# Optimization experiments

Measured on AMD Instinct MI355X. Metric: run time of the kernel, lower is better.

Reference implementation:

```python
import jax, jax.numpy as jnp
import numpy as np

B, T, D, H, F, E, K = 4, 1024, 1024, 16, 2048, 8, 2
LN_EPS = 1e-6  # flax LayerNorm default


def setup_inputs() -> dict:
    key = jax.random.key(0)
    ks = jax.random.split(key, 8)
    s = 0.02
    return {
        "x": jax.random.normal(ks[0], (B, T, D), jnp.float32),
        "ln1_scale": jnp.ones((D,), jnp.float32),
        "ln1_bias": jnp.zeros((D,), jnp.float32),
        "qkv_w": jax.random.normal(ks[1], (D, 3 * D), jnp.float32) * s,
        "qkv_b": jnp.zeros((3 * D,), jnp.float32),
        "out_w": jax.random.normal(ks[2], (D, D), jnp.float32) * s,
        "out_b": jnp.zeros((D,), jnp.float32),
        "ln2_scale": jnp.ones((D,), jnp.float32),
        "ln2_bias": jnp.zeros((D,), jnp.float32),
        "router_w": jax.random.normal(ks[3], (D, E), jnp.float32) * s,
        "w1": jax.random.normal(ks[4], (E, D, F), jnp.float32) * s,
        "b1": jnp.zeros((E, F), jnp.float32),
        "w2": jax.random.normal(ks[5], (E, F, D), jnp.float32) * s,
        "b2": jnp.zeros((E, D), jnp.float32),
    }


def _layernorm(x, scale, bias):
    mu = jnp.mean(x, axis=-1, keepdims=True)
    var = jnp.mean(jnp.square(x - mu), axis=-1, keepdims=True)
    return (x - mu) * jax.lax.rsqrt(var + LN_EPS) * scale + bias


def _attention(x, qkv_w, qkv_b, out_w, out_b):
    b, t, d = x.shape
    hd = d // H
    qkv = x @ qkv_w + qkv_b
    q, k, v = jnp.split(qkv, 3, axis=-1)
    q = q.reshape(b, t, H, hd).transpose(0, 2, 1, 3)  # (B,H,T,hd)
    k = k.reshape(b, t, H, hd).transpose(0, 2, 1, 3)
    v = v.reshape(b, t, H, hd).transpose(0, 2, 1, 3)
    scale = jnp.sqrt(jnp.float32(hd))
    scores = jnp.einsum("bhqd,bhkd->bhqk", q, k) / scale
    causal = jnp.triu(jnp.ones((t, t), jnp.bool_), k=1)
    scores = jnp.where(causal[None, None], -1e9, scores)
    attn = jax.nn.softmax(scores, axis=-1)
    out = jnp.einsum("bhqk,bhkd->bhqd", attn, v)
    out = out.transpose(0, 2, 1, 3).reshape(b, t, d)
    return out @ out_w + out_b


def _moe(x, router_w, w1, b1, w2, b2):
    b, t, d = x.shape
    logits = x @ router_w  # (B,T,E)
    probs = jax.nn.softmax(logits, axis=-1)
    topk_vals, topk_idx = jax.lax.top_k(logits, K)  # (B,T,K)
    gates = jax.nn.softmax(topk_vals, axis=-1)
    # aux load-balancing loss from top-1 dispatch
    dispatch = jax.nn.one_hot(topk_idx[..., 0], E, dtype=x.dtype)
    f = jnp.mean(dispatch, axis=(0, 1))
    P = jnp.mean(probs, axis=(0, 1))
    aux_loss = E * jnp.sum(f * P)
    # dense all-expert compute (faithful to original)
    h = jax.nn.gelu(jnp.einsum("btd,edf->ebtf", x, w1) + b1[:, None, None, :])
    eo = jnp.einsum("ebtf,efd->ebtd", h, w2) + b2[:, None, None, :]  # (E,B,T,D)
    bi = jnp.arange(b)[:, None, None]
    ti = jnp.arange(t)[None, :, None]
    selected = eo[topk_idx, bi, ti, :]  # (B,T,K,D)
    out = jnp.sum(gates[..., None] * selected, axis=2)
    return out, aux_loss


def reference(x, ln1_scale, ln1_bias, qkv_w, qkv_b, out_w, out_b,
              ln2_scale, ln2_bias, router_w, w1, b1, w2, b2):
    res = x
    h = _layernorm(x, ln1_scale, ln1_bias)
    h = _attention(h, qkv_w, qkv_b, out_w, out_b)
    x = h + res
    res = x
    hn = _layernorm(x, ln2_scale, ln2_bias)
    moe_out, aux_loss = _moe(hn, router_w, w1, b1, w2, b2)
    return moe_out + res, aux_loss
```

## Files before the change

kernel.cpp:

```cpp
#include <hip/hip_runtime.h>
#include <hip/hip_bf16.h>

using bf16 = __hip_bfloat16;
typedef __attribute__((ext_vector_type(8))) short short8;
typedef __attribute__((ext_vector_type(4))) float f32x4;

__device__ __forceinline__ unsigned short f2bu(float x) {
  union { bf16 b; unsigned short u; } cv; cv.b = __float2bfloat16(x); return cv.u;
}

__device__ __forceinline__ void gload_lds16(const bf16* g, bf16* l) {
  __builtin_amdgcn_global_load_lds(
      (const __attribute__((address_space(1))) void*)g,
      (__attribute__((address_space(3))) void*)l, 16, 0, 0);
}

__global__ __launch_bounds__(256) void transpose_to_bf16(
    const float* __restrict__ in, bf16* __restrict__ out, int R, int C) {
  __shared__ float tile[64][65];
  size_t bo = (size_t)blockIdx.z * R * C;
  in += bo; out += bo;
  int c0 = blockIdx.x * 64, r0 = blockIdx.y * 64;
  int tx = threadIdx.x & 15, ty = threadIdx.x >> 4;
#pragma unroll
  for (int i = 0; i < 4; ++i) {
    float4 v = *(const float4*)&in[(size_t)(r0 + ty + i * 16) * C + c0 + tx * 4];
    tile[ty + i * 16][tx * 4 + 0] = v.x;
    tile[ty + i * 16][tx * 4 + 1] = v.y;
    tile[ty + i * 16][tx * 4 + 2] = v.z;
    tile[ty + i * 16][tx * 4 + 3] = v.w;
  }
  __syncthreads();
  int c = threadIdx.x >> 2;
  int rg = (threadIdx.x & 3) * 16;
#pragma unroll
  for (int j = 0; j < 4; ++j) {
    ushort4 o;
    o.x = f2bu(tile[rg + j * 4 + 0][c]);
    o.y = f2bu(tile[rg + j * 4 + 1][c]);
    o.z = f2bu(tile[rg + j * 4 + 2][c]);
    o.w = f2bu(tile[rg + j * 4 + 3][c]);
    *(ushort4*)&out[(size_t)(c0 + c) * R + r0 + rg + j * 4] = o;
  }
}

__global__ __launch_bounds__(256) void ln_kernel(
    const float* __restrict__ in, const float* __restrict__ sc,
    const float* __restrict__ bi, bf16* __restrict__ out) {
  int row = blockIdx.x, tid = threadIdx.x;
  const float4* xr = (const float4*)(in + (size_t)row * 1024);
  float4 v = xr[tid];
  float s = v.x + v.y + v.z + v.w;
  float sq = v.x * v.x + v.y * v.y + v.z * v.z + v.w * v.w;
#pragma unroll
  for (int m = 1; m < 64; m <<= 1) { s += __shfl_xor(s, m); sq += __shfl_xor(sq, m); }
  __shared__ float red[8];
  int wid = tid >> 6, lane = tid & 63;
  if (lane == 0) { red[wid] = s; red[4 + wid] = sq; }
  __syncthreads();
  s = red[0] + red[1] + red[2] + red[3];
  sq = red[4] + red[5] + red[6] + red[7];
  float mu = s * (1.f / 1024.f);
  float rstd = rsqrtf(sq * (1.f / 1024.f) - mu * mu + 1e-6f);
  float4 scv = ((const float4*)sc)[tid];
  float4 biv = ((const float4*)bi)[tid];
  ushort4 ov;
  ov.x = f2bu((v.x - mu) * rstd * scv.x + biv.x);
  ov.y = f2bu((v.y - mu) * rstd * scv.y + biv.y);
  ov.z = f2bu((v.z - mu) * rstd * scv.z + biv.z);
  ov.w = f2bu((v.w - mu) * rstd * scv.w + biv.w);
  ((ushort4*)(out + (size_t)row * 1024))[tid] = ov;
}

template <int BM, int BN, int EPI, bool GATHER, bool GROUPED>
__global__ __launch_bounds__(256) void gemm_bt(
    const bf16* __restrict__ A, const bf16* __restrict__ B,
    const float* __restrict__ bias, const float* __restrict__ resid,
    void* __restrict__ C, bf16* __restrict__ VT, const int* __restrict__ gidx,
    const int* __restrict__ counts, const int* __restrict__ offsets,
    int M, int N, int K) {
  constexpr int FM = BM / 32;
  constexpr int FN = BN / 32;
  constexpr int AL = BM / 32;
  constexpr int BL = BN / 32;
  int e = blockIdx.z;
  int Mcnt = M, base = 0;
  if (GROUPED) { Mcnt = counts[e]; base = offsets[e]; }
  int m0 = blockIdx.y * BM, n0 = blockIdx.x * BN;
  if (m0 >= Mcnt) return;
  const bf16* Bp = B + (size_t)e * N * K;
  const float* biasp = bias + (size_t)e * N;
  __shared__ __align__(16) bf16 As[BM * 64];
  __shared__ __align__(16) bf16 Bs[BN * 64];
  int tid = threadIdx.x, lane = tid & 63, wid = tid >> 6;
  int lr = lane & 15, lg = lane >> 4;
  int wr = (wid >> 1) * (BM / 2), wc = (wid & 1) * (BN / 2);
  const bf16* aptr[AL];
  const bf16* bptr[BL];
  int adst[AL], bdst[BL];
#pragma unroll
  for (int i = 0; i < AL; ++i) {
    int idx = i * 256 + tid;
    int r = idx >> 3, cb = idx & 7;
    int cbs = cb ^ (r & 7);
    int gr = m0 + r;
    int cl = gr < Mcnt ? gr : (Mcnt - 1);
    size_t arow = GATHER ? (size_t)gidx[base + cl] : (size_t)(base + cl);
    aptr[i] = A + arow * K + cbs * 8;
    adst[i] = idx * 8;
  }
#pragma unroll
  for (int i = 0; i < BL; ++i) {
    int idx = i * 256 + tid;
    int r = idx >> 3, cb = idx & 7;
    int cbs = cb ^ (r & 7);
    bptr[i] = Bp + (size_t)(n0 + r) * K + cbs * 8;
    bdst[i] = idx * 8;
  }
  int xa = lr & 7;
  int colk[2];
  colk[0] = (lg ^ xa) * 8;
  colk[1] = ((lg + 4) ^ xa) * 8;
  int arow_lds[FM], brow_lds[FN];
#pragma unroll
  for (int m_ = 0; m_ < FM; ++m_) arow_lds[m_] = (wr + m_ * 16 + lr) * 64;
#pragma unroll
  for (int n_ = 0; n_ < FN; ++n_) brow_lds[n_] = (wc + n_ * 16 + lr) * 64;

  f32x4 acc[FM][FN] = {};
  int nt = K >> 6;
  for (int t = 0; t < nt; ++t) {
    __syncthreads();
    int k0 = t << 6;
#pragma unroll
    for (int i = 0; i < AL; ++i) gload_lds16(aptr[i] + k0, &As[adst[i]]);
#pragma unroll
    for (int i = 0; i < BL; ++i) gload_lds16(bptr[i] + k0, &Bs[bdst[i]]);
    __syncthreads();
#pragma unroll
    for (int h = 0; h < 2; ++h) {
      short8 af[FM], bfg[FN];
#pragma unroll
      for (int m_ = 0; m_ < FM; ++m_)
        af[m_] = *(const short8*)&As[arow_lds[m_] + colk[h]];
#pragma unroll
      for (int n_ = 0; n_ < FN; ++n_)
        bfg[n_] = *(const short8*)&Bs[brow_lds[n_] + colk[h]];
#pragma unroll
      for (int m_ = 0; m_ < FM; ++m_)
#pragma unroll
        for (int n_ = 0; n_ < FN; ++n_)
          acc[m_][n_] = __builtin_amdgcn_mfma_f32_16x16x32_bf16(af[m_], bfg[n_], acc[m_][n_], 0, 0, 0);
    }
  }
#pragma unroll
  for (int n_ = 0; n_ < FN; ++n_) {
    int acol = n0 + wc + n_ * 16 + lr;
    float bv = biasp[acol];
#pragma unroll
    for (int m_ = 0; m_ < FM; ++m_) {
      int rbase = m0 + wr + m_ * 16 + lg * 4;
#pragma unroll
      for (int q = 0; q < 4; ++q) {
        int gr = rbase + q;
        if (gr >= Mcnt) continue;
        size_t crow = (size_t)(base + gr);
        float v = acc[m_][n_][q] + bv;
        if (EPI == 1) {
          float z = 0.7978845608028654f * (v + 0.044715f * v * v * v);
          float t2 = __expf(2.f * z);
          v = v * (t2 / (t2 + 1.f));
          ((bf16*)C)[crow * N + acol] = __float2bfloat16(v);
        } else if (EPI == 2) {
          ((float*)C)[crow * N + acol] = v + resid[crow * N + acol];
        } else if (EPI == 3) {
          if (acol < 2048) {
            ((bf16*)C)[crow * N + acol] = __float2bfloat16(v);
          } else {
            int dg = acol - 2048;
            int hh = dg >> 6, dd = dg & 63;
            int bb = (int)(crow >> 10), tt = (int)(crow & 1023);
            VT[(((size_t)bb * 16 + hh) * 64 + dd) * 1024 + tt] = __float2bfloat16(v);
          }
        } else {
          ((bf16*)C)[crow * N + acol] = __float2bfloat16(v);
        }
      }
    }
  }
}

__global__ __launch_bounds__(256) void attn_kernel(const bf16* __restrict__ qkv,
                                                   const bf16* __restrict__ vt,
                                                   bf16* __restrict__ out) {
  constexpr int T = 1024, QS = 3072;
  int bh = blockIdx.y;
  int b = bh >> 4, h = bh & 15;
  __shared__ __align__(16) bf16 Ks[64][72];
  __shared__ __align__(16) bf16 Vs[64][72];
  __shared__ __align__(16) bf16 Pl[4][16][72];
  int tid = threadIdx.x, lane = tid & 63, wid = tid >> 6;
  int lr = lane & 15, lg = lane >> 4;
  const size_t rowb = (size_t)b * T;
  const float SC = 0.18033688011112042f;
  int sr[2], scb[2];
  const bf16* kbase[2];
  const bf16* vbase[2];
#pragma unroll
  for (int i = 0; i < 2; ++i) {
    int idx = tid + i * 256;
    sr[i] = idx >> 3; scb[i] = idx & 7;
    kbase[i] = qkv + (rowb + sr[i]) * QS + 1024 + h * 64 + scb[i] * 8;
    vbase[i] = vt + ((size_t)bh * 64 + sr[i]) * T + scb[i] * 8;
  }
  for (int half = 0; half < 2; ++half) {
    int qt = (half == 0) ? blockIdx.x : (15 - blockIdx.x);
    int qrow0 = qt * 64 + wid * 16 + lg * 4;
    const bf16* qp = qkv + (rowb + qt * 64 + wid * 16 + lr) * QS + h * 64;
    short8 qf0 = *(const short8*)(qp + lg * 8);
    short8 qf1 = *(const short8*)(qp + 32 + lg * 8);
    f32x4 o[4] = {};
    float mrow[4] = {-3e38f, -3e38f, -3e38f, -3e38f};
    float lrow[4] = {0.f, 0.f, 0.f, 0.f};
    short8 kreg[2], vreg[2];
#pragma unroll
    for (int i = 0; i < 2; ++i) {
      kreg[i] = *(const short8*)kbase[i];
      vreg[i] = *(const short8*)vbase[i];
    }
    for (int kv = 0; kv <= qt; ++kv) {
      __syncthreads();
#pragma unroll
      for (int i = 0; i < 2; ++i) {
        *(short8*)&Ks[sr[i]][scb[i] * 8] = kreg[i];
        *(short8*)&Vs[sr[i]][scb[i] * 8] = vreg[i];
      }
      __syncthreads();
      if (kv < qt) {
#pragma unroll
        for (int i = 0; i < 2; ++i) {
          kreg[i] = *(const short8*)(kbase[i] + (size_t)(kv + 1) * 64 * QS);
          vreg[i] = *(const short8*)(vbase[i] + (kv + 1) * 64);
        }
      }
      f32x4 s[4];
#pragma unroll
      for (int nf = 0; nf < 4; ++nf) {
        f32x4 z = {0.f, 0.f, 0.f, 0.f};
        short8 k0 = *(const short8*)&Ks[nf * 16 + lr][lg * 8];
        short8 k1 = *(const short8*)&Ks[nf * 16 + lr][32 + lg * 8];
        z = __builtin_amdgcn_mfma_f32_16x16x32_bf16(qf0, k0, z, 0, 0, 0);
        z = __builtin_amdgcn_mfma_f32_16x16x32_bf16(qf1, k1, z, 0, 0, 0);
        s[nf] = z;
      }
      bool diag = (kv == qt);
#pragma unroll
      for (int nf = 0; nf < 4; ++nf)
#pragma unroll
        for (int q = 0; q < 4; ++q) {
          float v = s[nf][q] * SC;
          if (diag) { int key = kv * 64 + nf * 16 + lr; if (key > qrow0 + q) v = -1e9f; }
          s[nf][q] = v;
        }
      float rs[4], resc[4];
#pragma unroll
      for (int q = 0; q < 4; ++q) {
        float v = fmaxf(fmaxf(s[0][q], s[1][q]), fmaxf(s[2][q], s[3][q]));
        v = fmaxf(v, __shfl_xor(v, 1));
        v = fmaxf(v, __shfl_xor(v, 2));
        v = fmaxf(v, __shfl_xor(v, 4));
        v = fmaxf(v, __shfl_xor(v, 8));
        float mn = fmaxf(mrow[q], v);
        resc[q] = __builtin_amdgcn_exp2f(mrow[q] - mn);
        mrow[q] = mn;
        rs[q] = 0.f;
      }
#pragma unroll
      for (int nf = 0; nf < 4; ++nf)
#pragma unroll
        for (int q = 0; q < 4; ++q) {
          float p = __builtin_amdgcn_exp2f(s[nf][q] - mrow[q]);
          rs[q] += p;
          Pl[wid][lg * 4 + q][nf * 16 + lr] = __float2bfloat16(p);
        }
#pragma unroll
      for (int q = 0; q < 4; ++q) {
        float v = rs[q];
        v += __shfl_xor(v, 1); v += __shfl_xor(v, 2);
        v += __shfl_xor(v, 4); v += __shfl_xor(v, 8);
        lrow[q] = lrow[q] * resc[q] + v;
        o[0][q] *= resc[q]; o[1][q] *= resc[q]; o[2][q] *= resc[q]; o[3][q] *= resc[q];
      }
      short8 pa0 = *(const short8*)&Pl[wid][lr][lg * 8];
      short8 pa1 = *(const short8*)&Pl[wid][lr][32 + lg * 8];
#pragma unroll
      for (int nf = 0; nf < 4; ++nf) {
        short8 v0 = *(const short8*)&Vs[nf * 16 + lr][lg * 8];
        short8 v1 = *(const short8*)&Vs[nf * 16 + lr][32 + lg * 8];
        o[nf] = __builtin_amdgcn_mfma_f32_16x16x32_bf16(pa0, v0, o[nf], 0, 0, 0);
        o[nf] = __builtin_amdgcn_mfma_f32_16x16x32_bf16(pa1, v1, o[nf], 0, 0, 0);
      }
    }
#pragma unroll
    for (int q = 0; q < 4; ++q) {
      float inv = 1.0f / lrow[q];
      size_t row = rowb + qrow0 + q;
#pragma unroll
      for (int nf = 0; nf < 4; ++nf)
        out[row * 1024 + h * 64 + nf * 16 + lr] = __float2bfloat16(o[nf][q] * inv);
    }
  }
}

__global__ __launch_bounds__(64) void router_kernel(
    const float* __restrict__ x2, const float* __restrict__ sc,
    const float* __restrict__ bi, const float* __restrict__ rw,
    bf16* __restrict__ ln2h, float* __restrict__ probs,
    int* __restrict__ topk, float* __restrict__ gates) {
  int t = blockIdx.x, lane = threadIdx.x;
  const float* xr = x2 + (size_t)t * 1024;
  float xv[16];
  float s = 0.f, sq = 0.f;
#pragma unroll
  for (int i = 0; i < 4; ++i) {
    float4 v = ((const float4*)xr)[lane * 4 + i];
    xv[i * 4 + 0] = v.x; xv[i * 4 + 1] = v.y; xv[i * 4 + 2] = v.z; xv[i * 4 + 3] = v.w;
    s += v.x + v.y + v.z + v.w;
    sq += v.x * v.x + v.y * v.y + v.z * v.z + v.w * v.w;
  }
#pragma unroll
  for (int m = 1; m < 64; m <<= 1) { s += __shfl_xor(s, m); sq += __shfl_xor(sq, m); }
  float mu = s * (1.f / 1024.f);
  float rstd = rsqrtf(sq * (1.f / 1024.f) - mu * mu + 1e-6f);
  float a8[8] = {};
  short8 o0, o1;
#pragma unroll
  for (int i = 0; i < 16; ++i) {
    int d = lane * 16 + i;
    float y = (xv[i] - mu) * rstd * sc[d] + bi[d];
    if (i < 8) o0[i] = (short)f2bu(y); else o1[i - 8] = (short)f2bu(y);
    const float4* rr = (const float4*)(rw + (size_t)d * 8);
    float4 r0 = rr[0], r1 = rr[1];
    a8[0] += y * r0.x; a8[1] += y * r0.y; a8[2] += y * r0.z; a8[3] += y * r0.w;
    a8[4] += y * r1.x; a8[5] += y * r1.y; a8[6] += y * r1.z; a8[7] += y * r1.w;
  }
  *(short8*)&ln2h[(size_t)t * 1024 + lane * 16] = o0;
  *(short8*)&ln2h[(size_t)t * 1024 + lane * 16 + 8] = o1;
#pragma unroll
  for (int m = 1; m < 64; m <<= 1)
#pragma unroll
    for (int e = 0; e < 8; ++e) a8[e] += __shfl_xor(a8[e], m);
  if (lane == 0) {
    float mx = a8[0];
#pragma unroll
    for (int e = 1; e < 8; ++e) mx = fmaxf(mx, a8[e]);
    float ps = 0.f, pe[8];
#pragma unroll
    for (int e = 0; e < 8; ++e) { pe[e] = expf(a8[e] - mx); ps += pe[e]; }
    float inv = 1.f / ps;
#pragma unroll
    for (int e = 0; e < 8; ++e) probs[t * 8 + e] = pe[e] * inv;
    int i0 = 0; float v0 = a8[0];
#pragma unroll
    for (int e = 1; e < 8; ++e) if (a8[e] > v0) { v0 = a8[e]; i0 = e; }
    int i1 = -1; float v1 = -3e38f;
#pragma unroll
    for (int e = 0; e < 8; ++e) if (e != i0 && a8[e] > v1) { v1 = a8[e]; i1 = e; }
    float g1 = 1.f / (1.f + expf(v0 - v1));
    topk[t * 2] = i0; topk[t * 2 + 1] = i1;
    gates[t * 2] = 1.f - g1; gates[t * 2 + 1] = g1;
  }
}

__global__ __launch_bounds__(256) void assign_kernel(
    const int* __restrict__ topk, int* __restrict__ counts,
    int* __restrict__ offsets, int* __restrict__ rows_tok,
    int* __restrict__ pair_pos) {
  int e = blockIdx.x;
  int tid = threadIdx.x, lane = tid & 63, wid = tid >> 6;
  __shared__ int c[8];
  if (tid < 8) c[tid] = 0;
  __syncthreads();
  for (int p = tid; p < 8192; p += 256) atomicAdd(&c[topk[p]], 1);
  __syncthreads();
  int base = 0;
  for (int k = 0; k < 8; ++k) if (k < e) base += c[k];
  if (tid == 0) { counts[e] = c[e]; offsets[e] = base; }
  __shared__ int wsum[4];
  int run = 0;
  for (int start = 0; start < 8192; start += 256) {
    int p = start + tid;
    int f = (topk[p] == e) ? 1 : 0;
    int v = f;
#pragma unroll
    for (int o_ = 1; o_ < 64; o_ <<= 1) { int u = __shfl_up(v, o_); if (lane >= o_) v += u; }
    if (lane == 63) wsum[wid] = v;
    __syncthreads();
    int wbase = 0;
#pragma unroll
    for (int w = 0; w < 4; ++w) if (w < wid) wbase += wsum[w];
    int tot = wsum[0] + wsum[1] + wsum[2] + wsum[3];
    if (f) {
      int pos = base + run + wbase + v - 1;
      rows_tok[pos] = p >> 1;
      pair_pos[p] = pos;
    }
    run += tot;
    __syncthreads();
  }
}

__global__ __launch_bounds__(256) void combine_kernel(
    const float* __restrict__ x2, const bf16* __restrict__ eo,
    const float* __restrict__ gates, const int* __restrict__ pair_pos,
    const float* __restrict__ probs, const int* __restrict__ topk,
    float* __restrict__ out, float* __restrict__ aux_out) {
  int t = blockIdx.x, tid = threadIdx.x;
  if (t == 4096) {
    int lane = tid & 63, wid = tid >> 6;
    float P[8] = {}, Fc[8] = {};
    for (int tt = tid; tt < 4096; tt += 256) {
#pragma unroll
      for (int e = 0; e < 8; ++e) P[e] += probs[tt * 8 + e];
      Fc[topk[tt * 2]] += 1.f;
    }
#pragma unroll
    for (int m = 1; m < 64; m <<= 1)
#pragma unroll
      for (int e = 0; e < 8; ++e) { P[e] += __shfl_xor(P[e], m); Fc[e] += __shfl_xor(Fc[e], m); }
    __shared__ float sP[4][8], sF[4][8];
    if (lane == 0)
#pragma unroll
      for (int e = 0; e < 8; ++e) { sP[wid][e] = P[e]; sF[wid][e] = Fc[e]; }
    __syncthreads();
    if (tid == 0) {
      float aux = 0.f;
      for (int e = 0; e < 8; ++e) {
        float p = (sP[0][e] + sP[1][e] + sP[2][e] + sP[3][e]) * (1.f / 4096.f);
        float f = (sF[0][e] + sF[1][e] + sF[2][e] + sF[3][e]) * (1.f / 4096.f);
        aux += f * p;
      }
      aux_out[0] = 8.f * aux;
    }
    return;
  }
  float g0 = gates[t * 2], g1 = gates[t * 2 + 1];
  size_t p0 = (size_t)pair_pos[t * 2] * 1024, p1 = (size_t)pair_pos[t * 2 + 1] * 1024;
  size_t rb = (size_t)t * 1024;
#pragma unroll
  for (int i = 0; i < 4; ++i) {
    int d = tid + i * 256;
    out[rb + d] = x2[rb + d] + g0 * __bfloat162float(eo[p0 + d]) + g1 * __bfloat162float(eo[p1 + d]);
  }
}

extern "C" void kernel_launch(void* const* d_in, const int* in_sizes, int n_in,
                              void* d_out, int out_size, void* d_ws, size_t ws_size,
                              hipStream_t stream) {
  (void)in_sizes; (void)n_in; (void)out_size; (void)ws_size;
  const float* x    = (const float*)d_in[0];
  const float* ln1s = (const float*)d_in[1];
  const float* ln1b = (const float*)d_in[2];
  const float* qkvw = (const float*)d_in[3];
  const float* qkvb = (const float*)d_in[4];
  const float* outw = (const float*)d_in[5];
  const float* outb = (const float*)d_in[6];
  const float* ln2s = (const float*)d_in[7];
  const float* ln2b = (const float*)d_in[8];
  const float* rw   = (const float*)d_in[9];
  const float* w1   = (const float*)d_in[10];
  const float* b1   = (const float*)d_in[11];
  const float* w2   = (const float*)d_in[12];
  const float* b2   = (const float*)d_in[13];

  char* ws = (char*)d_ws;
  size_t off = 0;
  auto alloc = [&](size_t bytes) -> char* {
    char* p = ws + off; off += (bytes + 255) & ~(size_t)255; return p;
  };
  bf16* qkvw_t  = (bf16*)alloc(3072ull * 1024 * 2);
  bf16* outw_t  = (bf16*)alloc(1024ull * 1024 * 2);
  bf16* w1_t    = (bf16*)alloc(8ull * 2048 * 1024 * 2);
  bf16* w2_t    = (bf16*)alloc(8ull * 1024 * 2048 * 2);
  bf16* h1      = (bf16*)alloc(4096ull * 1024 * 2);
  bf16* qkv     = (bf16*)alloc(4096ull * 3072 * 2);
  bf16* vtb     = (bf16*)alloc(64ull * 64 * 1024 * 2);
  bf16* attn_o  = (bf16*)alloc(4096ull * 1024 * 2);
  float* x2     = (float*)alloc(4096ull * 1024 * 4);
  bf16* ln2h    = (bf16*)alloc(4096ull * 1024 * 2);
  float* probs  = (float*)alloc(4096ull * 8 * 4);
  float* gates  = (float*)alloc(4096ull * 2 * 4);
  int* topk     = (int*)alloc(8192 * 4);
  int* counts   = (int*)alloc(64 * 4);
  int* offsets  = (int*)alloc(64 * 4);
  int* rows_tok = (int*)alloc(8192 * 4);
  int* pair_pos = (int*)alloc(8192 * 4);
  bf16* h_buf   = (bf16*)alloc(8192ull * 2048 * 2);
  bf16* eo      = (bf16*)alloc(8192ull * 1024 * 2);

  transpose_to_bf16<<<dim3(3072 / 64, 1024 / 64, 1), 256, 0, stream>>>(qkvw, qkvw_t, 1024, 3072);
  transpose_to_bf16<<<dim3(1024 / 64, 1024 / 64, 1), 256, 0, stream>>>(outw, outw_t, 1024, 1024);
  transpose_to_bf16<<<dim3(2048 / 64, 1024 / 64, 8), 256, 0, stream>>>(w1, w1_t, 1024, 2048);
  transpose_to_bf16<<<dim3(1024 / 64, 2048 / 64, 8), 256, 0, stream>>>(w2, w2_t, 2048, 1024);

  ln_kernel<<<4096, 256, 0, stream>>>(x, ln1s, ln1b, h1);

  gemm_bt<64, 128, 3, false, false><<<dim3(3072 / 128, 4096 / 64, 1), 256, 0, stream>>>(
      h1, qkvw_t, qkvb, nullptr, qkv, vtb, nullptr, nullptr, nullptr, 4096, 3072, 1024);

  attn_kernel<<<dim3(8, 64), 256, 0, stream>>>(qkv, vtb, attn_o);

  gemm_bt<64, 128, 2, false, false><<<dim3(1024 / 128, 4096 / 64, 1), 256, 0, stream>>>(
      attn_o, outw_t, outb, x, x2, nullptr, nullptr, nullptr, nullptr, 4096, 1024, 1024);

  router_kernel<<<4096, 64, 0, stream>>>(x2, ln2s, ln2b, rw, ln2h, probs, topk, gates);

  assign_kernel<<<8, 256, 0, stream>>>(topk, counts, offsets, rows_tok, pair_pos);

  gemm_bt<64, 128, 1, true, true><<<dim3(2048 / 128, 8192 / 64, 8), 256, 0, stream>>>(
      ln2h, w1_t, b1, nullptr, h_buf, nullptr, rows_tok, counts, offsets, 8192, 2048, 1024);

  gemm_bt<64, 128, 0, false, true><<<dim3(1024 / 128, 8192 / 64, 8), 256, 0, stream>>>(
      h_buf, w2_t, b2, nullptr, eo, nullptr, nullptr, counts, offsets, 8192, 1024, 2048);

  combine_kernel<<<4097, 256, 0, stream>>>(x2, eo, gates, pair_pos, probs, topk,
                                           (float*)d_out, (float*)d_out + 4194304);
}
```

Before: 357.5 us.

## Merge weight transposes into one launch and double attention KV tile

The four weight transpose/convert launches are merged into a single kernel that works out the matrix and tile from a flat block index, which removes three launch overheads. The attention kernel now stages 128 keys and values per iteration instead of 64 and processes them as two 64-key sub-steps. This halves the number of barrier pairs and global prefetch rounds per KV sweep. In exchange it doubles shared memory for K/V and the registers used for prefetch, and the causal mask check now runs on every sub-step.

```diff
diff --git a/kernel.cpp b/kernel.cpp
--- a/kernel.cpp
+++ b/kernel.cpp
@@ -15,12 +15,21 @@
       (__attribute__((address_space(3))) void*)l, 16, 0, 0);
 }
 
-__global__ __launch_bounds__(256) void transpose_to_bf16(
-    const float* __restrict__ in, bf16* __restrict__ out, int R, int C) {
+__global__ __launch_bounds__(256) void transpose4(
+    const float* __restrict__ i0, bf16* __restrict__ o0,
+    const float* __restrict__ i1, bf16* __restrict__ o1,
+    const float* __restrict__ i2, bf16* __restrict__ o2,
+    const float* __restrict__ i3, bf16* __restrict__ o3) {
   __shared__ float tile[64][65];
-  size_t bo = (size_t)blockIdx.z * R * C;
+  int bid = blockIdx.x;
+  const float* in; bf16* out; int R, C, bx, by, bz = 0;
+  if (bid < 768)        { in = i0; out = o0; R = 1024; C = 3072; bx = bid % 48; by = bid / 48; }
+  else if (bid < 1024)  { int b = bid - 768;  in = i1; out = o1; R = 1024; C = 1024; bx = b % 16; by = b / 16; }
+  else if (bid < 5120)  { int b = bid - 1024; in = i2; out = o2; R = 1024; C = 2048; bz = b >> 9; int lb = b & 511; bx = lb % 32; by = lb / 32; }
+  else                  { int b = bid - 5120; in = i3; out = o3; R = 2048; C = 1024; bz = b >> 9; int lb = b & 511; bx = lb % 16; by = lb / 16; }
+  size_t bo = (size_t)bz * R * C;
   in += bo; out += bo;
-  int c0 = blockIdx.x * 64, r0 = blockIdx.y * 64;
+  int c0 = bx * 64, r0 = by * 64;
   int tx = threadIdx.x & 15, ty = threadIdx.x >> 4;
 #pragma unroll
   for (int i = 0; i < 4; ++i) {
@@ -196,109 +205,118 @@
   constexpr int T = 1024, QS = 3072;
   int bh = blockIdx.y;
   int b = bh >> 4, h = bh & 15;
-  __shared__ __align__(16) bf16 Ks[64][72];
-  __shared__ __align__(16) bf16 Vs[64][72];
+  __shared__ __align__(16) bf16 Ks[128][72];
+  __shared__ __align__(16) bf16 Vs[64][136];
   __shared__ __align__(16) bf16 Pl[4][16][72];
   int tid = threadIdx.x, lane = tid & 63, wid = tid >> 6;
   int lr = lane & 15, lg = lane >> 4;
   const size_t rowb = (size_t)b * T;
   const float SC = 0.18033688011112042f;
-  int sr[2], scb[2];
-  const bf16* kbase[2];
-  const bf16* vbase[2];
-#pragma unroll
-  for (int i = 0; i < 2; ++i) {
+  int ksr[4], kscb[4];
+  const bf16* kbase[4];
+  int vr[4], vc[4];
+  const bf16* vbase[4];
+#pragma unroll
+  for (int i = 0; i < 4; ++i) {
     int idx = tid + i * 256;
-    sr[i] = idx >> 3; scb[i] = idx & 7;
-    kbase[i] = qkv + (rowb + sr[i]) * QS + 1024 + h * 64 + scb[i] * 8;
-    vbase[i] = vt + ((size_t)bh * 64 + sr[i]) * T + scb[i] * 8;
+    ksr[i] = idx >> 3; kscb[i] = idx & 7;
+    kbase[i] = qkv + (rowb + ksr[i]) * QS + 1024 + h * 64 + kscb[i] * 8;
+    vr[i] = idx >> 4; vc[i] = idx & 15;
+    vbase[i] = vt + ((size_t)bh * 64 + vr[i]) * T + vc[i] * 8;
   }
   for (int half = 0; half < 2; ++half) {
     int qt = (half == 0) ? blockIdx.x : (15 - blockIdx.x);
     int qrow0 = qt * 64 + wid * 16 + lg * 4;
+    int qmax = qt * 64 + 63;
     const bf16* qp = qkv + (rowb + qt * 64 + wid * 16 + lr) * QS + h * 64;
     short8 qf0 = *(const short8*)(qp + lg * 8);
     short8 qf1 = *(const short8*)(qp + 32 + lg * 8);
     f32x4 o[4] = {};
     float mrow[4] = {-3e38f, -3e38f, -3e38f, -3e38f};
     float lrow[4] = {0.f, 0.f, 0.f, 0.f};
-    short8 kreg[2], vreg[2];
-#pragma unroll
-    for (int i = 0; i < 2; ++i) {
+    int nkvb = (qt >> 1) + 1;
+    short8 kreg[4], vreg[4];
+#pragma unroll
+    for (int i = 0; i < 4; ++i) {
       kreg[i] = *(const short8*)kbase[i];
       vreg[i] = *(const short8*)vbase[i];
     }
-    for (int kv = 0; kv <= qt; ++kv) {
+    for (int kvb = 0; kvb < nkvb; ++kvb) {
       __syncthreads();
 #pragma unroll
-      for (int i = 0; i < 2; ++i) {
-        *(short8*)&Ks[sr[i]][scb[i] * 8] = kreg[i];
-        *(short8*)&Vs[sr[i]][scb[i] * 8] = vreg[i];
+      for (int i = 0; i < 4; ++i) {
+        *(short8*)&Ks[ksr[i]][kscb[i] * 8] = kreg[i];
+        *(short8*)&Vs[vr[i]][vc[i] * 8] = vreg[i];
       }
       __syncthreads();
-      if (kv < qt) {
-#pragma unroll
-        for (int i = 0; i < 2; ++i) {
-          kreg[i] = *(const short8*)(kbase[i] + (size_t)(kv + 1) * 64 * QS);
-          vreg[i] = *(const short8*)(vbase[i] + (kv + 1) * 64);
+      if (kvb + 1 < nkvb) {
+#pragma unroll
+        for (int i = 0; i < 4; ++i) {
+          kreg[i] = *(const short8*)(kbase[i] + (size_t)(kvb + 1) * 128 * QS);
+          vreg[i] = *(const short8*)(vbase[i] + (kvb + 1) * 128);
         }
       }
-      f32x4 s[4];
-#pragma unroll
-      for (int nf = 0; nf < 4; ++nf) {
-        f32x4 z = {0.f, 0.f, 0.f, 0.f};
-        short8 k0 = *(const short8*)&Ks[nf * 16 + lr][lg * 8];
-        short8 k1 = *(const short8*)&Ks[nf * 16 + lr][32 + lg * 8];
-        z = __builtin_amdgcn_mfma_f32_16x16x32_bf16(qf0, k0, z, 0, 0, 0);
-        z = __builtin_amdgcn_mfma_f32_16x16x32_bf16(qf1, k1, z, 0, 0, 0);
-        s[nf] = z;
-      }
-      bool diag = (kv == qt);
-#pragma unroll
-      for (int nf = 0; nf < 4; ++nf)
+#pragma unroll
+      for (int hs = 0; hs < 2; ++hs) {
+        int kb0 = kvb * 128 + hs * 64;
+        if (kb0 > qmax) break;
+        f32x4 s[4];
+#pragma unroll
+        for (int nf = 0; nf < 4; ++nf) {
+          f32x4 z = {0.f, 0.f, 0.f, 0.f};
+          short8 k0 = *(const short8*)&Ks[hs * 64 + nf * 16 + lr][lg * 8];
+          short8 k1 = *(const short8*)&Ks[hs * 64 + nf * 16 + lr][32 + lg * 8];
+          z = __builtin_amdgcn_mfma_f32_16x16x32_bf16(qf0, k0, z, 0, 0, 0);
+          z = __builtin_amdgcn_mfma_f32_16x16x32_bf16(qf1, k1, z, 0, 0, 0);
+          s[nf] = z;
+        }
+#pragma unroll
+        for (int nf = 0; nf < 4; ++nf)
+#pragma unroll
+          for (int q = 0; q < 4; ++q) {
+            float v = s[nf][q] * SC;
+            int key = kb0 + nf * 16 + lr;
+            if (key > qrow0 + q) v = -1e9f;
+            s[nf][q] = v;
+          }
+        float rs[4], resc[4];
 #pragma unroll
         for (int q = 0; q < 4; ++q) {
-          float v = s[nf][q] * SC;
-          if (diag) { int key = kv * 64 + nf * 16 + lr; if (key > qrow0 + q) v = -1e9f; }
-          s[nf][q] = v;
+          float v = fmaxf(fmaxf(s[0][q], s[1][q]), fmaxf(s[2][q], s[3][q]));
+          v = fmaxf(v, __shfl_xor(v, 1));
+          v = fmaxf(v, __shfl_xor(v, 2));
+          v = fmaxf(v, __shfl_xor(v, 4));
+          v = fmaxf(v, __shfl_xor(v, 8));
+          float mn = fmaxf(mrow[q], v);
+          resc[q] = __builtin_amdgcn_exp2f(mrow[q] - mn);
+          mrow[q] = mn;
+          rs[q] = 0.f;
         }
-      float rs[4], resc[4];
-#pragma unroll
-      for (int q = 0; q < 4; ++q) {
-        float v = fmaxf(fmaxf(s[0][q], s[1][q]), fmaxf(s[2][q], s[3][q]));
-        v = fmaxf(v, __shfl_xor(v, 1));
-        v = fmaxf(v, __shfl_xor(v, 2));
-        v = fmaxf(v, __shfl_xor(v, 4));
-        v = fmaxf(v, __shfl_xor(v, 8));
-        float mn = fmaxf(mrow[q], v);
-        resc[q] = __builtin_amdgcn_exp2f(mrow[q] - mn);
-        mrow[q] = mn;
-        rs[q] = 0.f;
-      }
-#pragma unroll
-      for (int nf = 0; nf < 4; ++nf)
+#pragma unroll
+        for (int nf = 0; nf < 4; ++nf)
+#pragma unroll
+          for (int q = 0; q < 4; ++q) {
+            float p = __builtin_amdgcn_exp2f(s[nf][q] - mrow[q]);
+            rs[q] += p;
+            Pl[wid][lg * 4 + q][nf * 16 + lr] = __float2bfloat16(p);
+          }
 #pragma unroll
         for (int q = 0; q < 4; ++q) {
-          float p = __builtin_amdgcn_exp2f(s[nf][q] - mrow[q]);
-          rs[q] += p;
-          Pl[wid][lg * 4 + q][nf * 16 + lr] = __float2bfloat16(p);
+          float v = rs[q];
+          v += __shfl_xor(v, 1); v += __shfl_xor(v, 2);
+          v += __shfl_xor(v, 4); v += __shfl_xor(v, 8);
+          lrow[q] = lrow[q] * resc[q] + v;
+          o[0][q] *= resc[q]; o[1][q] *= resc[q]; o[2][q] *= resc[q]; o[3][q] *= resc[q];
         }
-#pragma unroll
-      for (int q = 0; q < 4; ++q) {
-        float v = rs[q];
-        v += __shfl_xor(v, 1); v += __shfl_xor(v, 2);
-        v += __shfl_xor(v, 4); v += __shfl_xor(v, 8);
-        lrow[q] = lrow[q] * resc[q] + v;
-        o[0][q] *= resc[q]; o[1][q] *= resc[q]; o[2][q] *= resc[q]; o[3][q] *= resc[q];
-      }
-      short8 pa0 = *(const short8*)&Pl[wid][lr][lg * 8];
-      short8 pa1 = *(const short8*)&Pl[wid][lr][32 + lg * 8];
-#pragma unroll
-      for (int nf = 0; nf < 4; ++nf) {
-        short8 v0 = *(const short8*)&Vs[nf * 16 + lr][lg * 8];
-        short8 v1 = *(const short8*)&Vs[nf * 16 + lr][32 + lg * 8];
-        o[nf] = __builtin_amdgcn_mfma_f32_16x16x32_bf16(pa0, v0, o[nf], 0, 0, 0);
-        o[nf] = __builtin_amdgcn_mfma_f32_16x16x32_bf16(pa1, v1, o[nf], 0, 0, 0);
+        short8 pa0 = *(const short8*)&Pl[wid][lr][lg * 8];
+        short8 pa1 = *(const short8*)&Pl[wid][lr][32 + lg * 8];
+#pragma unroll
+        for (int nf = 0; nf < 4; ++nf) {
+          short8 v0 = *(const short8*)&Vs[nf * 16 + lr][hs * 64 + lg * 8];
+          short8 v1 = *(const short8*)&Vs[nf * 16 + lr][hs * 64 + 32 + lg * 8];
+          o[nf] = __builtin_amdgcn_mfma_f32_16x16x32_bf16(pa0, v0, o[nf], 0, 0, 0);
+          o[nf] = __builtin_amdgcn_mfma_f32_16x16x32_bf16(pa1, v1, o[nf], 0, 0, 0);
+        }
       }
     }
 #pragma unroll
@@ -498,10 +516,7 @@
   bf16* h_buf   = (bf16*)alloc(8192ull * 2048 * 2);
   bf16* eo      = (bf16*)alloc(8192ull * 1024 * 2);
 
-  transpose_to_bf16<<<dim3(3072 / 64, 1024 / 64, 1), 256, 0, stream>>>(qkvw, qkvw_t, 1024, 3072);
-  transpose_to_bf16<<<dim3(1024 / 64, 1024 / 64, 1), 256, 0, stream>>>(outw, outw_t, 1024, 1024);
-  transpose_to_bf16<<<dim3(2048 / 64, 1024 / 64, 8), 256, 0, stream>>>(w1, w1_t, 1024, 2048);
-  transpose_to_bf16<<<dim3(1024 / 64, 2048 / 64, 8), 256, 0, stream>>>(w2, w2_t, 2048, 1024);
+  transpose4<<<9216, 256, 0, stream>>>(qkvw, qkvw_t, outw, outw_t, w1, w1_t, w2, w2_t);
 
   ln_kernel<<<4096, 256, 0, stream>>>(x, ln1s, ln1b, h1);
 
```

Result: faster. 350.3 us (-2.0%).
